# Kernel tuning notes

Measured on AMD Instinct MI355X. Metric: run time of the kernel, lower is better.

## Reference

```python
import jax, jax.numpy as jnp
import numpy as np

B, A, D, H = 2048, 32, 128, 256

def setup_inputs() -> dict:
    key = jax.random.key(0)
    ks = jax.random.split(key, 12)
    s = lambda fan_in: 1.0 / np.sqrt(fan_in)
    return {
        "obs": jax.random.normal(ks[0], (B, A, D), dtype=jnp.float32),
        "act": jax.random.normal(ks[1], (B, A, 8), dtype=jnp.float32),
        "enc_W": jax.random.uniform(ks[2], (H, D), jnp.float32, -s(D), s(D)),
        "enc_b": jax.random.uniform(ks[3], (H,), jnp.float32, -s(D), s(D)),
        "fobs_W": jax.random.uniform(ks[4], (H, H), jnp.float32, -s(H), s(H)),
        "fobs_b": jax.random.uniform(ks[5], (H,), jnp.float32, -s(H), s(H)),
        "W_ih": jax.random.uniform(ks[6], (3 * H, H), jnp.float32, -s(H), s(H)),
        "b_ih": jax.random.uniform(ks[7], (3 * H,), jnp.float32, -s(H), s(H)),
        "W_hh": jax.random.uniform(ks[8], (3 * H, H), jnp.float32, -s(H), s(H)),
        "b_hh": jax.random.uniform(ks[9], (3 * H,), jnp.float32, -s(H), s(H)),
        "dec_W": jax.random.uniform(ks[10], (1, H), jnp.float32, -s(H), s(H)),
        "dec_b": jax.random.uniform(ks[11], (1,), jnp.float32, -s(H), s(H)),
    }

def _gru_cell(x, h, W_ih, b_ih, W_hh, b_hh):
    # torch.nn.GRUCell: gates stacked as [reset, update, new]
    gi = x @ W_ih.T + b_ih          # [N, 3H]
    gh = h @ W_hh.T + b_hh          # [N, 3H]
    i_r, i_z, i_n = jnp.split(gi, 3, axis=-1)
    h_r, h_z, h_n = jnp.split(gh, 3, axis=-1)
    r = jax.nn.sigmoid(i_r + h_r)
    z = jax.nn.sigmoid(i_z + h_z)
    n = jnp.tanh(i_n + r * h_n)
    return (1.0 - z) * n + z * h

def reference(obs, act, enc_W, enc_b, fobs_W, fobs_b, W_ih, b_ih, W_hh, b_hh, dec_W, dec_b):
    b, a, d = obs.shape
    x = obs.reshape(b * a, d)                         # [B*A, D]
    e = jax.nn.relu(x @ enc_W.T + enc_b)              # encoder + ReLU
    h = e @ fobs_W.T + fobs_b                         # h_out
    # k = 0: comm input is zeros
    h = _gru_cell(jnp.zeros_like(h), h, W_ih, b_ih, W_hh, b_hh)
    # k = 1: masked mean over other agents == (sum_j h_j - h_i) / n_agents
    hA = h.reshape(b, a, -1)                          # [B, A, H]
    c = (hA.sum(axis=1, keepdims=True) - hA) / a      # [B, A, H]
    h = _gru_cell(c.reshape(b * a, -1), h, W_ih, b_ih, W_hh, b_hh)
    return (h @ dec_W.T + dec_b).reshape(b, a, -1)    # [B, A, 1]
```

## Files before the change

kernel.cpp:

```cpp
#include <hip/hip_runtime.h>
#include <hip/hip_fp16.h>


#define NB   2048
#define NA   32
#define DIN  128
#define HID  256
#define SA   264
#define MROWS 64

typedef _Float16 half8  __attribute__((ext_vector_type(8)));
typedef float    float4v __attribute__((ext_vector_type(4)));

#define ENC_OFF    0
#define FOBS_OFF   32768
#define WIH_OFF    98304
#define WHH_OFF    294912
#define PREP_TOTAL 491520

__global__ void prep_weights(const float* __restrict__ encW, const float* __restrict__ fobsW,
                             const float* __restrict__ wih,  const float* __restrict__ whh,
                             _Float16* __restrict__ prep) {
    int F = blockIdx.x * 256 + threadIdx.x;
    if (F >= PREP_TOTAL) return;
    const float* src; int K, NT, local = F;
    if (F < FOBS_OFF)     { src = encW;  K = 128; NT = 16; }
    else if (F < WIH_OFF) { src = fobsW; K = 256; NT = 16; local = F - FOBS_OFF; }
    else if (F < WHH_OFF) { src = wih;   K = 256; NT = 48; local = F - WIH_OFF; }
    else                  { src = whh;   K = 256; NT = 48; local = F - WHH_OFF; }
    int j    = local & 7;
    int lane = (local >> 3) & 63;
    int t    = local >> 9;
    int nt   = t % NT;
    int ks   = t / NT;
    int col  = nt * 16 + (lane & 15);
    int k    = ks * 32 + ((lane >> 4) << 3) + j;
    prep[F] = (_Float16)src[col * K + k];
}

__device__ __forceinline__ float sigmoid_f(float x) {
    x = fminf(fmaxf(x, -30.f), 30.f);
    return 1.f / (1.f + __expf(-x));
}
__device__ __forceinline__ float tanh_f(float x) {
    x = fminf(fmaxf(x, -15.f), 15.f);
    float e = __expf(-2.f * x);
    return (1.f - e) / (1.f + e);
}

__device__ __forceinline__ half8 ldB(const _Float16* __restrict__ prepm, int NT, int nt, int ks,
                                     const float* __restrict__ raw, int K, int use_prep, int lane) {
    if (use_prep)
        return *(const half8*)(prepm + (((ks * NT + nt) * 64 + lane) << 3));
    half8 b;
    int l16 = lane & 15, kq = (lane >> 4) << 3;
    #pragma unroll
    for (int j = 0; j < 8; j++)
        b[j] = (_Float16)raw[(nt * 16 + l16) * K + ks * 32 + kq + j];
    return b;
}

template<int KSTEPS>
__device__ __forceinline__ void gemm_col16(const _Float16* __restrict__ Abuf,
        const _Float16* __restrict__ prepm, int NT, int nt,
        const float* __restrict__ raw, int K, int use_prep,
        int lane, float4v acc[4])
{
    const int l16 = lane & 15;
    const int kq  = (lane >> 4) << 3;
    #pragma unroll 2
    for (int ks = 0; ks < KSTEPS; ks++) {
        int kbase = ks * 32 + kq;
        half8 Af[4];
        #pragma unroll
        for (int mt = 0; mt < 4; mt++)
            Af[mt] = *(const half8*)(Abuf + (mt * 16 + l16) * SA + kbase);
        half8 b0 = ldB(prepm, NT, nt, ks, raw, K, use_prep, lane);
        #pragma unroll
        for (int mt = 0; mt < 4; mt++)
            acc[mt] = __builtin_amdgcn_mfma_f32_16x16x32_f16(Af[mt], b0, acc[mt], 0, 0, 0);
    }
}

__global__ __launch_bounds__(1024, 4) void commnet_fused(
    const float* __restrict__ obs, const _Float16* __restrict__ prep,
    const float* __restrict__ enc_b, const float* __restrict__ fobs_b,
    const float* __restrict__ b_ih, const float* __restrict__ b_hh,
    const float* __restrict__ dec_W, const float* __restrict__ dec_b,
    float* __restrict__ out,
    const float* __restrict__ encW, const float* __restrict__ fobsW,
    const float* __restrict__ wih, const float* __restrict__ whh,
    int use_prep)
{
    const int b    = blockIdx.x;
    const int tid  = threadIdx.x;
    const int lane = tid & 63;
    const int w    = tid >> 6;
    const int l16  = lane & 15;
    const int quad = lane >> 4;
    const int kq   = quad << 3;
    const int col  = w * 16 + l16;

    __shared__ __align__(16) _Float16 sA[2][MROWS * SA];
    __shared__ __align__(16) float S[2][HID];
    __shared__ float Srow[MROWS];

    {
        const float* obsb = obs + (size_t)b * MROWS * DIN;
        int r   = tid >> 4;
        int off = (tid & 15) << 3;
        const float* src = obsb + r * DIN + off;
        float4v v0 = *(const float4v*)(src);
        float4v v1 = *(const float4v*)(src + 4);
        half8 hv;
        hv[0] = (_Float16)v0[0]; hv[1] = (_Float16)v0[1];
        hv[2] = (_Float16)v0[2]; hv[3] = (_Float16)v0[3];
        hv[4] = (_Float16)v1[0]; hv[5] = (_Float16)v1[1];
        hv[6] = (_Float16)v1[2]; hv[7] = (_Float16)v1[3];
        *(half8*)(&sA[0][r * SA + off]) = hv;
    }
    __syncthreads();

    float4v acc[4];

    {
        float4v z = {0.f, 0.f, 0.f, 0.f};
        acc[0] = z; acc[1] = z; acc[2] = z; acc[3] = z;
        gemm_col16<4>(&sA[0][0], prep + ENC_OFF, 16, w, encW, DIN, use_prep, lane, acc);
        float bb = enc_b[col];
        #pragma unroll
        for (int mt = 0; mt < 4; mt++)
            #pragma unroll
            for (int r = 0; r < 4; r++) {
                int row = mt * 16 + quad * 4 + r;
                sA[1][row * SA + col] = (_Float16)fmaxf(acc[mt][r] + bb, 0.f);
            }
    }
    __syncthreads();

    {
        float4v z = {0.f, 0.f, 0.f, 0.f};
        acc[0] = z; acc[1] = z; acc[2] = z; acc[3] = z;
        gemm_col16<8>(&sA[1][0], prep + FOBS_OFF, 16, w, fobsW, HID, use_prep, lane, acc);
        float bb = fobs_b[col];
        #pragma unroll
        for (int mt = 0; mt < 4; mt++)
            #pragma unroll
            for (int r = 0; r < 4; r++) {
                int row = mt * 16 + quad * 4 + r;
                sA[0][row * SA + col] = (_Float16)(acc[mt][r] + bb);
            }
    }
    __syncthreads();

    {
        float4v aR[4], aZ[4], aN[4];
        float4v z = {0.f, 0.f, 0.f, 0.f};
        #pragma unroll
        for (int mt = 0; mt < 4; mt++) { aR[mt] = z; aZ[mt] = z; aN[mt] = z; }
        #pragma unroll 2
        for (int ks = 0; ks < 8; ks++) {
            const int kbase = ks * 32 + kq;
            half8 Af[4];
            #pragma unroll
            for (int mt = 0; mt < 4; mt++)
                Af[mt] = *(const half8*)(&sA[0][(mt * 16 + l16) * SA + kbase]);
            half8 bR = ldB(prep + WHH_OFF, 48,  0 + w, ks, whh, HID, use_prep, lane);
            half8 bZ = ldB(prep + WHH_OFF, 48, 16 + w, ks, whh, HID, use_prep, lane);
            half8 bN = ldB(prep + WHH_OFF, 48, 32 + w, ks, whh, HID, use_prep, lane);
            #pragma unroll
            for (int mt = 0; mt < 4; mt++)
                aR[mt] = __builtin_amdgcn_mfma_f32_16x16x32_f16(Af[mt], bR, aR[mt], 0, 0, 0);
            #pragma unroll
            for (int mt = 0; mt < 4; mt++)
                aZ[mt] = __builtin_amdgcn_mfma_f32_16x16x32_f16(Af[mt], bZ, aZ[mt], 0, 0, 0);
            #pragma unroll
            for (int mt = 0; mt < 4; mt++)
                aN[mt] = __builtin_amdgcn_mfma_f32_16x16x32_f16(Af[mt], bN, aN[mt], 0, 0, 0);
        }
        float biR = b_ih[col],       bhR = b_hh[col];
        float biZ = b_ih[256 + col], bhZ = b_hh[256 + col];
        float biN = b_ih[512 + col], bhN = b_hh[512 + col];
        float s0 = 0.f, s1 = 0.f;
        #pragma unroll
        for (int mt = 0; mt < 4; mt++) {
            float psum = 0.f;
            #pragma unroll
            for (int r = 0; r < 4; r++) {
                int row = mt * 16 + quad * 4 + r;
                float rg = sigmoid_f(biR + aR[mt][r] + bhR);
                float zg = sigmoid_f(biZ + aZ[mt][r] + bhZ);
                float ng = tanh_f(biN + rg * (aN[mt][r] + bhN));
                float hold = (float)sA[0][row * SA + col];
                float h1 = (1.f - zg) * ng + zg * hold;
                sA[1][row * SA + col] = (_Float16)h1;
                psum += h1;
            }
            if (mt < 2) s0 += psum; else s1 += psum;
        }
        s0 += __shfl_xor(s0, 16); s0 += __shfl_xor(s0, 32);
        s1 += __shfl_xor(s1, 16); s1 += __shfl_xor(s1, 32);
        if (lane < 16) { S[0][col] = s0; S[1][col] = s1; }
    }
    __syncthreads();

    {
        #pragma unroll
        for (int it = 0; it < 2; it++) {
            int i  = tid + it * 1024;
            int r  = i >> 5;
            int c8 = (i & 31) << 3;
            const float* Sp = &S[r >> 5][0];
            half8 hv = *(const half8*)(&sA[1][r * SA + c8]);
            float4v t0 = *(const float4v*)(Sp + c8);
            float4v t1 = *(const float4v*)(Sp + c8 + 4);
            half8 cv;
            cv[0] = (_Float16)((t0[0] - (float)hv[0]) * (1.f / 32.f));
            cv[1] = (_Float16)((t0[1] - (float)hv[1]) * (1.f / 32.f));
            cv[2] = (_Float16)((t0[2] - (float)hv[2]) * (1.f / 32.f));
            cv[3] = (_Float16)((t0[3] - (float)hv[3]) * (1.f / 32.f));
            cv[4] = (_Float16)((t1[0] - (float)hv[4]) * (1.f / 32.f));
            cv[5] = (_Float16)((t1[1] - (float)hv[5]) * (1.f / 32.f));
            cv[6] = (_Float16)((t1[2] - (float)hv[6]) * (1.f / 32.f));
            cv[7] = (_Float16)((t1[3] - (float)hv[7]) * (1.f / 32.f));
            *(half8*)(&sA[0][r * SA + c8]) = cv;
        }
        if (tid < MROWS) Srow[tid] = 0.f;
    }
    __syncthreads();

    {
        float4v aR[4], aZ[4], aNi[4], aNh[4];
        float4v z = {0.f, 0.f, 0.f, 0.f};
        #pragma unroll
        for (int mt = 0; mt < 4; mt++) { aR[mt] = z; aZ[mt] = z; aNi[mt] = z; aNh[mt] = z; }
        #pragma unroll 2
        for (int ks = 0; ks < 8; ks++) {
            const int kbase = ks * 32 + kq;
            {
                half8 Cf[4];
                #pragma unroll
                for (int mt = 0; mt < 4; mt++)
                    Cf[mt] = *(const half8*)(&sA[0][(mt * 16 + l16) * SA + kbase]);
                half8 bR = ldB(prep + WIH_OFF, 48,  0 + w, ks, wih, HID, use_prep, lane);
                half8 bZ = ldB(prep + WIH_OFF, 48, 16 + w, ks, wih, HID, use_prep, lane);
                half8 bN = ldB(prep + WIH_OFF, 48, 32 + w, ks, wih, HID, use_prep, lane);
                #pragma unroll
                for (int mt = 0; mt < 4; mt++)
                    aR[mt]  = __builtin_amdgcn_mfma_f32_16x16x32_f16(Cf[mt], bR, aR[mt], 0, 0, 0);
                #pragma unroll
                for (int mt = 0; mt < 4; mt++)
                    aZ[mt]  = __builtin_amdgcn_mfma_f32_16x16x32_f16(Cf[mt], bZ, aZ[mt], 0, 0, 0);
                #pragma unroll
                for (int mt = 0; mt < 4; mt++)
                    aNi[mt] = __builtin_amdgcn_mfma_f32_16x16x32_f16(Cf[mt], bN, aNi[mt], 0, 0, 0);
            }
            {
                half8 Hf[4];
                #pragma unroll
                for (int mt = 0; mt < 4; mt++)
                    Hf[mt] = *(const half8*)(&sA[1][(mt * 16 + l16) * SA + kbase]);
                half8 bR = ldB(prep + WHH_OFF, 48,  0 + w, ks, whh, HID, use_prep, lane);
                half8 bZ = ldB(prep + WHH_OFF, 48, 16 + w, ks, whh, HID, use_prep, lane);
                half8 bN = ldB(prep + WHH_OFF, 48, 32 + w, ks, whh, HID, use_prep, lane);
                #pragma unroll
                for (int mt = 0; mt < 4; mt++)
                    aR[mt]  = __builtin_amdgcn_mfma_f32_16x16x32_f16(Hf[mt], bR, aR[mt], 0, 0, 0);
                #pragma unroll
                for (int mt = 0; mt < 4; mt++)
                    aZ[mt]  = __builtin_amdgcn_mfma_f32_16x16x32_f16(Hf[mt], bZ, aZ[mt], 0, 0, 0);
                #pragma unroll
                for (int mt = 0; mt < 4; mt++)
                    aNh[mt] = __builtin_amdgcn_mfma_f32_16x16x32_f16(Hf[mt], bN, aNh[mt], 0, 0, 0);
            }
        }

        float biR = b_ih[col],       bhR = b_hh[col];
        float biZ = b_ih[256 + col], bhZ = b_hh[256 + col];
        float biN = b_ih[512 + col], bhN = b_hh[512 + col];
        float dw  = dec_W[col];
        float p[4][4];
        #pragma unroll
        for (int mt = 0; mt < 4; mt++)
            #pragma unroll
            for (int r = 0; r < 4; r++) {
                int row = mt * 16 + quad * 4 + r;
                float rg = sigmoid_f(aR[mt][r] + biR + bhR);
                float zg = sigmoid_f(aZ[mt][r] + biZ + bhZ);
                float ng = tanh_f((aNi[mt][r] + biN) + rg * (aNh[mt][r] + bhN));
                float h1v = (float)sA[1][row * SA + col];
                float h2 = (1.f - zg) * ng + zg * h1v;
                p[mt][r] = h2 * dw;
            }
        #pragma unroll
        for (int m = 1; m <= 8; m <<= 1) {
            #pragma unroll
            for (int mt = 0; mt < 4; mt++)
                #pragma unroll
                for (int r = 0; r < 4; r++)
                    p[mt][r] += __shfl_xor(p[mt][r], m);
        }
        if (l16 == 0) {
            #pragma unroll
            for (int mt = 0; mt < 4; mt++)
                #pragma unroll
                for (int r = 0; r < 4; r++)
                    atomicAdd(&Srow[mt * 16 + quad * 4 + r], p[mt][r]);
        }
    }
    __syncthreads();
    if (tid < MROWS) out[(size_t)b * MROWS + tid] = Srow[tid] + dec_b[0];
}

extern "C" void kernel_launch(void* const* d_in, const int* in_sizes, int n_in,
                              void* d_out, int out_size, void* d_ws, size_t ws_size,
                              hipStream_t stream) {
    const float* obs   = (const float*)d_in[0];
    const float* encW  = (const float*)d_in[2];
    const float* encb  = (const float*)d_in[3];
    const float* fobsW = (const float*)d_in[4];
    const float* fobsb = (const float*)d_in[5];
    const float* wih   = (const float*)d_in[6];
    const float* bih   = (const float*)d_in[7];
    const float* whh   = (const float*)d_in[8];
    const float* bhh   = (const float*)d_in[9];
    const float* decW  = (const float*)d_in[10];
    const float* decb  = (const float*)d_in[11];
    float* out = (float*)d_out;

    _Float16* prep = (_Float16*)d_ws;
    int use_prep = (ws_size >= (size_t)PREP_TOTAL * sizeof(_Float16)) ? 1 : 0;
    if (use_prep) {
        prep_weights<<<(PREP_TOTAL + 255) / 256, 256, 0, stream>>>(encW, fobsW, wih, whh, prep);
    }
    commnet_fused<<<NB / 2, 1024, 0, stream>>>(obs, prep, encb, fobsb, bih, bhh, decW, decb, out,
                                               encW, fobsW, wih, whh, use_prep);
}
```

Baseline: 245.7 us.

## Halve block size and give each wave two column tiles

The fused kernel now launches 512 threads per block instead of 1024, so each wave covers two 16-column tiles. In the encoder and fobs GEMMs, each A fragment read from LDS now feeds two MFMAs. In the GRU phases the two tiles run one after another in a non-unrolled loop, and the second GRU's k-loop unrolling drops to 1. The aim is to cut LDS A-fragment traffic and register pressure per wave, but with LDS per block unchanged there are fewer resident waves per CU to hide latency.

```diff
diff --git a/kernel.cpp b/kernel.cpp
--- a/kernel.cpp
+++ b/kernel.cpp
@@ -60,29 +60,7 @@
     return b;
 }
 
-template<int KSTEPS>
-__device__ __forceinline__ void gemm_col16(const _Float16* __restrict__ Abuf,
-        const _Float16* __restrict__ prepm, int NT, int nt,
-        const float* __restrict__ raw, int K, int use_prep,
-        int lane, float4v acc[4])
-{
-    const int l16 = lane & 15;
-    const int kq  = (lane >> 4) << 3;
-    #pragma unroll 2
-    for (int ks = 0; ks < KSTEPS; ks++) {
-        int kbase = ks * 32 + kq;
-        half8 Af[4];
-        #pragma unroll
-        for (int mt = 0; mt < 4; mt++)
-            Af[mt] = *(const half8*)(Abuf + (mt * 16 + l16) * SA + kbase);
-        half8 b0 = ldB(prepm, NT, nt, ks, raw, K, use_prep, lane);
-        #pragma unroll
-        for (int mt = 0; mt < 4; mt++)
-            acc[mt] = __builtin_amdgcn_mfma_f32_16x16x32_f16(Af[mt], b0, acc[mt], 0, 0, 0);
-    }
-}
-
-__global__ __launch_bounds__(1024, 4) void commnet_fused(
+__global__ __launch_bounds__(512) void commnet_fused(
     const float* __restrict__ obs, const _Float16* __restrict__ prep,
     const float* __restrict__ enc_b, const float* __restrict__ fobs_b,
     const float* __restrict__ b_ih, const float* __restrict__ b_hh,
@@ -99,7 +77,7 @@
     const int l16  = lane & 15;
     const int quad = lane >> 4;
     const int kq   = quad << 3;
-    const int col  = w * 16 + l16;
+    const int nt0  = w * 2;
 
     __shared__ __align__(16) _Float16 sA[2][MROWS * SA];
     __shared__ __align__(16) float S[2][HID];
@@ -107,53 +85,97 @@
 
     {
         const float* obsb = obs + (size_t)b * MROWS * DIN;
-        int r   = tid >> 4;
-        int off = (tid & 15) << 3;
-        const float* src = obsb + r * DIN + off;
-        float4v v0 = *(const float4v*)(src);
-        float4v v1 = *(const float4v*)(src + 4);
-        half8 hv;
-        hv[0] = (_Float16)v0[0]; hv[1] = (_Float16)v0[1];
-        hv[2] = (_Float16)v0[2]; hv[3] = (_Float16)v0[3];
-        hv[4] = (_Float16)v1[0]; hv[5] = (_Float16)v1[1];
-        hv[6] = (_Float16)v1[2]; hv[7] = (_Float16)v1[3];
-        *(half8*)(&sA[0][r * SA + off]) = hv;
-    }
-    __syncthreads();
-
-    float4v acc[4];
+        #pragma unroll
+        for (int it = 0; it < 2; it++) {
+            int i   = tid + it * 512;
+            int r   = i >> 4;
+            int off = (i & 15) << 3;
+            const float* src = obsb + r * DIN + off;
+            float4v v0 = *(const float4v*)(src);
+            float4v v1 = *(const float4v*)(src + 4);
+            half8 hv;
+            hv[0] = (_Float16)v0[0]; hv[1] = (_Float16)v0[1];
+            hv[2] = (_Float16)v0[2]; hv[3] = (_Float16)v0[3];
+            hv[4] = (_Float16)v1[0]; hv[5] = (_Float16)v1[1];
+            hv[6] = (_Float16)v1[2]; hv[7] = (_Float16)v1[3];
+            *(half8*)(&sA[0][r * SA + off]) = hv;
+        }
+    }
+    __syncthreads();
 
     {
+        float4v acc[4][2];
         float4v z = {0.f, 0.f, 0.f, 0.f};
-        acc[0] = z; acc[1] = z; acc[2] = z; acc[3] = z;
-        gemm_col16<4>(&sA[0][0], prep + ENC_OFF, 16, w, encW, DIN, use_prep, lane, acc);
-        float bb = enc_b[col];
-        #pragma unroll
-        for (int mt = 0; mt < 4; mt++)
-            #pragma unroll
-            for (int r = 0; r < 4; r++) {
-                int row = mt * 16 + quad * 4 + r;
-                sA[1][row * SA + col] = (_Float16)fmaxf(acc[mt][r] + bb, 0.f);
-            }
+        #pragma unroll
+        for (int mt = 0; mt < 4; mt++) { acc[mt][0] = z; acc[mt][1] = z; }
+        #pragma unroll
+        for (int ks = 0; ks < 4; ks++) {
+            int kbase = ks * 32 + kq;
+            half8 Af[4];
+            #pragma unroll
+            for (int mt = 0; mt < 4; mt++)
+                Af[mt] = *(const half8*)(&sA[0][(mt * 16 + l16) * SA + kbase]);
+            half8 b0 = ldB(prep + ENC_OFF, 16, nt0,     ks, encW, DIN, use_prep, lane);
+            half8 b1 = ldB(prep + ENC_OFF, 16, nt0 + 1, ks, encW, DIN, use_prep, lane);
+            #pragma unroll
+            for (int mt = 0; mt < 4; mt++) {
+                acc[mt][0] = __builtin_amdgcn_mfma_f32_16x16x32_f16(Af[mt], b0, acc[mt][0], 0, 0, 0);
+                acc[mt][1] = __builtin_amdgcn_mfma_f32_16x16x32_f16(Af[mt], b1, acc[mt][1], 0, 0, 0);
+            }
+        }
+        #pragma unroll
+        for (int nt = 0; nt < 2; nt++) {
+            int col = (nt0 + nt) * 16 + l16;
+            float bb = enc_b[col];
+            #pragma unroll
+            for (int mt = 0; mt < 4; mt++)
+                #pragma unroll
+                for (int r = 0; r < 4; r++) {
+                    int row = mt * 16 + quad * 4 + r;
+                    sA[1][row * SA + col] = (_Float16)fmaxf(acc[mt][nt][r] + bb, 0.f);
+                }
+        }
     }
     __syncthreads();
 
     {
+        float4v acc[4][2];
         float4v z = {0.f, 0.f, 0.f, 0.f};
-        acc[0] = z; acc[1] = z; acc[2] = z; acc[3] = z;
-        gemm_col16<8>(&sA[1][0], prep + FOBS_OFF, 16, w, fobsW, HID, use_prep, lane, acc);
-        float bb = fobs_b[col];
-        #pragma unroll
-        for (int mt = 0; mt < 4; mt++)
-            #pragma unroll
-            for (int r = 0; r < 4; r++) {
-                int row = mt * 16 + quad * 4 + r;
-                sA[0][row * SA + col] = (_Float16)(acc[mt][r] + bb);
-            }
-    }
-    __syncthreads();
-
-    {
+        #pragma unroll
+        for (int mt = 0; mt < 4; mt++) { acc[mt][0] = z; acc[mt][1] = z; }
+        #pragma unroll 2
+        for (int ks = 0; ks < 8; ks++) {
+            int kbase = ks * 32 + kq;
+            half8 Af[4];
+            #pragma unroll
+            for (int mt = 0; mt < 4; mt++)
+                Af[mt] = *(const half8*)(&sA[1][(mt * 16 + l16) * SA + kbase]);
+            half8 b0 = ldB(prep + FOBS_OFF, 16, nt0,     ks, fobsW, HID, use_prep, lane);
+            half8 b1 = ldB(prep + FOBS_OFF, 16, nt0 + 1, ks, fobsW, HID, use_prep, lane);
+            #pragma unroll
+            for (int mt = 0; mt < 4; mt++) {
+                acc[mt][0] = __builtin_amdgcn_mfma_f32_16x16x32_f16(Af[mt], b0, acc[mt][0], 0, 0, 0);
+                acc[mt][1] = __builtin_amdgcn_mfma_f32_16x16x32_f16(Af[mt], b1, acc[mt][1], 0, 0, 0);
+            }
+        }
+        #pragma unroll
+        for (int nt = 0; nt < 2; nt++) {
+            int col = (nt0 + nt) * 16 + l16;
+            float bb = fobs_b[col];
+            #pragma unroll
+            for (int mt = 0; mt < 4; mt++)
+                #pragma unroll
+                for (int r = 0; r < 4; r++) {
+                    int row = mt * 16 + quad * 4 + r;
+                    sA[0][row * SA + col] = (_Float16)(acc[mt][nt][r] + bb);
+                }
+        }
+    }
+    __syncthreads();
+
+    #pragma unroll 1
+    for (int ps = 0; ps < 2; ps++) {
+        const int nt = nt0 + ps;
         float4v aR[4], aZ[4], aN[4];
         float4v z = {0.f, 0.f, 0.f, 0.f};
         #pragma unroll
@@ -165,9 +187,9 @@
             #pragma unroll
             for (int mt = 0; mt < 4; mt++)
                 Af[mt] = *(const half8*)(&sA[0][(mt * 16 + l16) * SA + kbase]);
-            half8 bR = ldB(prep + WHH_OFF, 48,  0 + w, ks, whh, HID, use_prep, lane);
-            half8 bZ = ldB(prep + WHH_OFF, 48, 16 + w, ks, whh, HID, use_prep, lane);
-            half8 bN = ldB(prep + WHH_OFF, 48, 32 + w, ks, whh, HID, use_prep, lane);
+            half8 bR = ldB(prep + WHH_OFF, 48,  0 + nt, ks, whh, HID, use_prep, lane);
+            half8 bZ = ldB(prep + WHH_OFF, 48, 16 + nt, ks, whh, HID, use_prep, lane);
+            half8 bN = ldB(prep + WHH_OFF, 48, 32 + nt, ks, whh, HID, use_prep, lane);
             #pragma unroll
             for (int mt = 0; mt < 4; mt++)
                 aR[mt] = __builtin_amdgcn_mfma_f32_16x16x32_f16(Af[mt], bR, aR[mt], 0, 0, 0);
@@ -178,6 +200,7 @@
             for (int mt = 0; mt < 4; mt++)
                 aN[mt] = __builtin_amdgcn_mfma_f32_16x16x32_f16(Af[mt], bN, aN[mt], 0, 0, 0);
         }
+        int col = nt * 16 + l16;
         float biR = b_ih[col],       bhR = b_hh[col];
         float biZ = b_ih[256 + col], bhZ = b_hh[256 + col];
         float biN = b_ih[512 + col], bhN = b_hh[512 + col];
@@ -200,14 +223,14 @@
         }
         s0 += __shfl_xor(s0, 16); s0 += __shfl_xor(s0, 32);
         s1 += __shfl_xor(s1, 16); s1 += __shfl_xor(s1, 32);
-        if (lane < 16) { S[0][col] = s0; S[1][col] = s1; }
+        if (lane < 16) { S[0][nt * 16 + lane] = s0; S[1][nt * 16 + lane] = s1; }
     }
     __syncthreads();
 
     {
         #pragma unroll
-        for (int it = 0; it < 2; it++) {
-            int i  = tid + it * 1024;
+        for (int it = 0; it < 4; it++) {
+            int i  = tid + it * 512;
             int r  = i >> 5;
             int c8 = (i & 31) << 3;
             const float* Sp = &S[r >> 5][0];
@@ -229,12 +252,14 @@
     }
     __syncthreads();
 
-    {
+    #pragma unroll 1
+    for (int ps = 0; ps < 2; ps++) {
+        const int nt = nt0 + ps;
         float4v aR[4], aZ[4], aNi[4], aNh[4];
         float4v z = {0.f, 0.f, 0.f, 0.f};
         #pragma unroll
         for (int mt = 0; mt < 4; mt++) { aR[mt] = z; aZ[mt] = z; aNi[mt] = z; aNh[mt] = z; }
-        #pragma unroll 2
+        #pragma unroll 1
         for (int ks = 0; ks < 8; ks++) {
             const int kbase = ks * 32 + kq;
             {
@@ -242,9 +267,9 @@
                 #pragma unroll
                 for (int mt = 0; mt < 4; mt++)
                     Cf[mt] = *(const half8*)(&sA[0][(mt * 16 + l16) * SA + kbase]);
-                half8 bR = ldB(prep + WIH_OFF, 48,  0 + w, ks, wih, HID, use_prep, lane);
-                half8 bZ = ldB(prep + WIH_OFF, 48, 16 + w, ks, wih, HID, use_prep, lane);
-                half8 bN = ldB(prep + WIH_OFF, 48, 32 + w, ks, wih, HID, use_prep, lane);
+                half8 bR = ldB(prep + WIH_OFF, 48,  0 + nt, ks, wih, HID, use_prep, lane);
+                half8 bZ = ldB(prep + WIH_OFF, 48, 16 + nt, ks, wih, HID, use_prep, lane);
+                half8 bN = ldB(prep + WIH_OFF, 48, 32 + nt, ks, wih, HID, use_prep, lane);
                 #pragma unroll
                 for (int mt = 0; mt < 4; mt++)
                     aR[mt]  = __builtin_amdgcn_mfma_f32_16x16x32_f16(Cf[mt], bR, aR[mt], 0, 0, 0);
@@ -260,9 +285,9 @@
                 #pragma unroll
                 for (int mt = 0; mt < 4; mt++)
                     Hf[mt] = *(const half8*)(&sA[1][(mt * 16 + l16) * SA + kbase]);
-                half8 bR = ldB(prep + WHH_OFF, 48,  0 + w, ks, whh, HID, use_prep, lane);
-                half8 bZ = ldB(prep + WHH_OFF, 48, 16 + w, ks, whh, HID, use_prep, lane);
-                half8 bN = ldB(prep + WHH_OFF, 48, 32 + w, ks, whh, HID, use_prep, lane);
+                half8 bR = ldB(prep + WHH_OFF, 48,  0 + nt, ks, whh, HID, use_prep, lane);
+                half8 bZ = ldB(prep + WHH_OFF, 48, 16 + nt, ks, whh, HID, use_prep, lane);
+                half8 bN = ldB(prep + WHH_OFF, 48, 32 + nt, ks, whh, HID, use_prep, lane);
                 #pragma unroll
                 for (int mt = 0; mt < 4; mt++)
                     aR[mt]  = __builtin_amdgcn_mfma_f32_16x16x32_f16(Hf[mt], bR, aR[mt], 0, 0, 0);
@@ -275,6 +300,7 @@
             }
         }
 
+        int col = nt * 16 + l16;
         float biR = b_ih[col],       bhR = b_hh[col];
         float biZ = b_ih[256 + col], bhZ = b_hh[256 + col];
         float biN = b_ih[512 + col], bhN = b_hh[512 + col];
@@ -333,6 +359,6 @@
     if (use_prep) {
         prep_weights<<<(PREP_TOTAL + 255) / 256, 256, 0, stream>>>(encW, fobsW, wih, whh, prep);
     }
-    commnet_fused<<<NB / 2, 1024, 0, stream>>>(obs, prep, encb, fobsb, bih, bhh, decW, decb, out,
-                                               encW, fobsW, wih, whh, use_prep);
-}
+    commnet_fused<<<NB / 2, 512, 0, stream>>>(obs, prep, encb, fobsb, bih, bhh, decW, decb, out,
+                                              encW, fobsW, wih, whh, use_prep);
+}
```

Result: faster. 236.4 us (-3.8%).
